# Optimization experiments

Hardware: AMD Instinct MI355X
Metric: run time of the kernel (lower is better)

## Reference

```python
import jax, jax.numpy as jnp
import numpy as np

DELTA_VAR = 0.5
DELTA_DIST = 1.5
VAR_WEIGHT = 1.0
DIST_WEIGHT = 1.0
REG_WEIGHT = 0.001
K = 16  # number of clusters (labels are in [0, K))


def setup_inputs() -> dict:
    key = jax.random.key(0)
    k1, k2 = jax.random.split(key)
    data = jax.random.normal(k1, (32, 512, 1024), dtype=jnp.float32)
    labels = jax.random.randint(k2, (512, 1024), 0, K, dtype=jnp.int32)
    return {"data": data, "labels": labels}


def reference(data, labels):
    D = data.shape[0]
    pts = data.reshape(D, -1).T          # [N, D] per-pixel embeddings
    lab = labels.reshape(-1)             # [N]

    # Per-cluster size and mean (center). All K clusters are present.
    counts = jax.ops.segment_sum(jnp.ones_like(lab, dtype=pts.dtype), lab,
                                 num_segments=K)          # [K]
    sums = jax.ops.segment_sum(pts, lab, num_segments=K)  # [K, D]
    centers = sums / counts[:, None]                      # [K, D]

    # Variance term: sum over all points of hinge(||center - x|| - dv)^2 / K
    diff = centers[lab] - pts                             # [N, D]
    dist = jnp.sqrt(jnp.sum(diff * diff, axis=-1))        # [N]
    var_term = jnp.sum(jnp.maximum(dist - DELTA_VAR, 0.0) ** 2) / K

    # Distance term: ordered pairs i != j of hinge(2*dd - ||ci - cj||)^2
    cd = centers[:, None, :] - centers[None, :, :]        # [K, K, D]
    sq = jnp.sum(cd * cd, axis=-1)                        # [K, K]
    eye = jnp.eye(K, dtype=bool)
    pd = jnp.sqrt(jnp.where(eye, 1.0, sq))                # safe sqrt on diag
    hinge = jnp.where(eye, 0.0, jnp.maximum(2.0 * DELTA_DIST - pd, 0.0) ** 2)
    dist_term = jnp.sum(hinge) / (K * (K - 1))

    # Regularization term: mean center norm
    reg_term = jnp.sum(jnp.sqrt(jnp.sum(centers * centers, axis=-1))) / K

    return VAR_WEIGHT * var_term + DIST_WEIGHT * dist_term + REG_WEIGHT * reg_term
```

## Files before the change

kernel.cpp:

```cpp
#include <hip/hip_runtime.h>


constexpr int KC = 16;
constexpr int DD = 32;
constexpr int NN = 512 * 1024;
constexpr int N4 = NN / 4;
constexpr int CHUNKS = 32;
constexpr int GROUPS_PER_CHUNK = N4 / CHUNKS;
constexpr int K1_ITERS = GROUPS_PER_CHUNK / 256;

constexpr int WS_P  = 0;
constexpr int WS_CP = 16384;

__global__ __launch_bounds__(256) void kA_sums(const float4* __restrict__ data4,
                                               const int4* __restrict__ lab4,
                                               float* __restrict__ ws,
                                               float* __restrict__ out) {
    const int tid = threadIdx.x;
    const int chunk = blockIdx.x;
    const int d = blockIdx.y;
    const bool doCnt = (d == 0);

    if (chunk == 0 && d == 0 && tid == 0) out[0] = 0.f;

    __shared__ float acc[KC * 256];
    __shared__ float cnt[KC * 256];
#pragma unroll
    for (int k = 0; k < KC; ++k) acc[k * 256 + tid] = 0.f;
    if (doCnt) {
#pragma unroll
        for (int k = 0; k < KC; ++k) cnt[k * 256 + tid] = 0.f;
    }
    __syncthreads();

    const int c0 = tid;
    const int c1 = (tid + 64) & 255;
    const int c2 = (tid + 128) & 255;
    const int c3 = (tid + 192) & 255;

    const float4* dplane = data4 + (size_t)d * N4;
    int g = chunk * GROUPS_PER_CHUNK + tid;

    float4 v = dplane[g];
    int4 lb = lab4[g];
    for (int it = 0; it < K1_ITERS; ++it) {
        float4 vn;
        int4 lbn;
        if (it + 1 < K1_ITERS) {
            vn = dplane[g + 256];
            lbn = lab4[g + 256];
        }
        const int i0 = lb.x * 256 + c0;
        const int i1 = lb.y * 256 + c1;
        const int i2 = lb.z * 256 + c2;
        const int i3 = lb.w * 256 + c3;
        const float a0 = acc[i0];
        const float a1 = acc[i1];
        const float a2 = acc[i2];
        const float a3 = acc[i3];
        acc[i0] = a0 + v.x;
        acc[i1] = a1 + v.y;
        acc[i2] = a2 + v.z;
        acc[i3] = a3 + v.w;
        if (doCnt) {
            const float b0 = cnt[i0];
            const float b1 = cnt[i1];
            const float b2 = cnt[i2];
            const float b3 = cnt[i3];
            cnt[i0] = b0 + 1.f;
            cnt[i1] = b1 + 1.f;
            cnt[i2] = b2 + 1.f;
            cnt[i3] = b3 + 1.f;
        }
        v = vn;
        lb = lbn;
        g += 256;
    }
    __syncthreads();

    const int k = tid >> 4, seg = tid & 15;
    float s = 0.f;
#pragma unroll
    for (int i = 0; i < 16; ++i) s += acc[k * 256 + seg * 16 + i];
#pragma unroll
    for (int off = 8; off > 0; off >>= 1) s += __shfl_down(s, off, 16);
    if (seg == 0) ws[WS_P + (k * DD + d) * CHUNKS + chunk] = s;
    if (doCnt) {
        float c = 0.f;
#pragma unroll
        for (int i = 0; i < 16; ++i) c += cnt[k * 256 + seg * 16 + i];
#pragma unroll
        for (int off = 8; off > 0; off >>= 1) c += __shfl_down(c, off, 16);
        if (seg == 0) ws[WS_CP + k * CHUNKS + chunk] = c;
    }
}

__global__ __launch_bounds__(256) void kB_var(const float4* __restrict__ data4,
                                              const int4* __restrict__ lab4,
                                              const float* __restrict__ ws,
                                              float* __restrict__ out) {
    __shared__ float csum[KC * 33];
    __shared__ float ccnt[KC];
    __shared__ float ct2[DD * 32];
    const int tid = threadIdx.x;

    {
        int idx = tid;
        const float* p = ws + WS_P + idx * CHUNKS;
        float s = 0.f;
#pragma unroll
        for (int c = 0; c < CHUNKS; ++c) s += p[c];
        csum[(idx >> 5) * 33 + (idx & 31)] = s;
        idx = tid + 256;
        p = ws + WS_P + idx * CHUNKS;
        s = 0.f;
#pragma unroll
        for (int c = 0; c < CHUNKS; ++c) s += p[c];
        csum[(idx >> 5) * 33 + (idx & 31)] = s;
    }
    if (tid < KC) {
        const float* p = ws + WS_CP + tid * CHUNKS;
        float c = 0.f;
#pragma unroll
        for (int i = 0; i < CHUNKS; ++i) c += p[i];
        ccnt[tid] = c;
    }
    __syncthreads();

    for (int idx = tid; idx < KC * DD; idx += 256) {
        const int k = idx >> 5, d = idx & 31;
        const float c = csum[k * 33 + d] / ccnt[k];
        ct2[d * 32 + k] = c;
        ct2[d * 32 + 16 + k] = c;
    }
    __syncthreads();

    if (blockIdx.x == 0) {
        const int i = tid >> 4, j = tid & 15;
        float val;
        if (i != j) {
            float sq = 0.f;
#pragma unroll
            for (int d = 0; d < DD; ++d) {
                const float df = ct2[d * 32 + i] - ct2[d * 32 + j];
                sq += df * df;
            }
            const float pd = sqrtf(sq);
            const float t = fmaxf(3.0f - pd, 0.f);
            val = t * t * (1.0f / (KC * (KC - 1)));
        } else {
            float s2 = 0.f;
#pragma unroll
            for (int d = 0; d < DD; ++d) s2 += ct2[d * 32 + i] * ct2[d * 32 + i];
            val = sqrtf(s2) * (0.001f / KC);
        }
        __shared__ float red[256];
        red[tid] = val;
        __syncthreads();
        for (int off = 128; off > 0; off >>= 1) {
            if (tid < off) red[tid] += red[tid + off];
            __syncthreads();
        }
        if (tid == 0) atomicAdd(out, red[0]);
        __syncthreads();
    }

    const int g = blockIdx.x * 256 + tid;
    const int4 lb = lab4[g];
    const int dup = (tid & 32) >> 1;
    const int o0 = lb.x + dup, o1 = lb.y + dup, o2 = lb.z + dup, o3 = lb.w + dup;

    float s0 = 0.f, s1 = 0.f, s2 = 0.f, s3 = 0.f;
#pragma unroll 8
    for (int d = 0; d < DD; ++d) {
        const float4 v = data4[(size_t)d * N4 + g];
        const float* ctd = ct2 + d * 32;
        const float d0 = ctd[o0] - v.x; s0 += d0 * d0;
        const float d1 = ctd[o1] - v.y; s1 += d1 * d1;
        const float d2 = ctd[o2] - v.z; s2 += d2 * d2;
        const float d3 = ctd[o3] - v.w; s3 += d3 * d3;
    }
    const float h0 = fmaxf(sqrtf(s0) - 0.5f, 0.f);
    const float h1 = fmaxf(sqrtf(s1) - 0.5f, 0.f);
    const float h2 = fmaxf(sqrtf(s2) - 0.5f, 0.f);
    const float h3 = fmaxf(sqrtf(s3) - 0.5f, 0.f);
    float lsum = h0 * h0 + h1 * h1 + h2 * h2 + h3 * h3;

#pragma unroll
    for (int off = 32; off > 0; off >>= 1) lsum += __shfl_down(lsum, off);
    __shared__ float wred[4];
    if ((tid & 63) == 0) wred[tid >> 6] = lsum;
    __syncthreads();
    if (tid == 0) {
        const float s = wred[0] + wred[1] + wred[2] + wred[3];
        atomicAdd(out, s * (1.0f / KC));
    }
}

extern "C" void kernel_launch(void* const* d_in, const int* in_sizes, int n_in,
                              void* d_out, int out_size, void* d_ws, size_t ws_size,
                              hipStream_t stream) {
    const float4* data4 = (const float4*)d_in[0];
    const int4* lab4 = (const int4*)d_in[1];
    float* out = (float*)d_out;
    float* ws = (float*)d_ws;

    kA_sums<<<dim3(CHUNKS, DD), 256, 0, stream>>>(data4, lab4, ws, out);
    kB_var<<<512, 256, 0, stream>>>(data4, lab4, ws, out);
}
```

Baseline: 111.9 us.

## Split count blocks out, use atomic partial sums, and halve per-block work in variance kernel

Kernel A now uses 64 chunks per dimension and moves label counting into 32 dedicated blocks, which frees the d==0 blocks from the extra count scatter and halves shared memory per block. Partial sums go through global atomics into a padded workspace that is zeroed by a memset, replacing the per-chunk arrays that kernel B had to reduce. Kernel B splits the 32 dimensions across two thread halves that combine through shared memory, doubling the block count so more loads are in flight. The costs are an extra memset launch, atomic contention, and nondeterministic float summation order.

```diff
diff --git a/kernel.cpp b/kernel.cpp
--- a/kernel.cpp
+++ b/kernel.cpp
@@ -5,32 +5,29 @@
 constexpr int DD = 32;
 constexpr int NN = 512 * 1024;
 constexpr int N4 = NN / 4;
-constexpr int CHUNKS = 32;
-constexpr int GROUPS_PER_CHUNK = N4 / CHUNKS;
-constexpr int K1_ITERS = GROUPS_PER_CHUNK / 256;
-
-constexpr int WS_P  = 0;
-constexpr int WS_CP = 16384;
+constexpr int CHUNKS = 64;
+constexpr int GPC = N4 / CHUNKS;
+constexpr int AITERS = GPC / 256;
+constexpr int NDATA = CHUNKS * DD;
+constexpr int NCNT = 32;
+constexpr int CITERS = N4 / NCNT / 256;
+
+constexpr int WS_SUM = 0;
+constexpr int WS_CNT = 8192;
+constexpr int WS_ZERO_FLOATS = 8448;
 
 __global__ __launch_bounds__(256) void kA_sums(const float4* __restrict__ data4,
                                                const int4* __restrict__ lab4,
                                                float* __restrict__ ws,
                                                float* __restrict__ out) {
     const int tid = threadIdx.x;
-    const int chunk = blockIdx.x;
-    const int d = blockIdx.y;
-    const bool doCnt = (d == 0);
-
-    if (chunk == 0 && d == 0 && tid == 0) out[0] = 0.f;
+    const int bid = blockIdx.x;
+
+    if (bid == 0 && tid == 0) out[0] = 0.f;
 
     __shared__ float acc[KC * 256];
-    __shared__ float cnt[KC * 256];
 #pragma unroll
     for (int k = 0; k < KC; ++k) acc[k * 256 + tid] = 0.f;
-    if (doCnt) {
-#pragma unroll
-        for (int k = 0; k < KC; ++k) cnt[k * 256 + tid] = 0.f;
-    }
     __syncthreads();
 
     const int c0 = tid;
@@ -38,60 +35,78 @@
     const int c2 = (tid + 128) & 255;
     const int c3 = (tid + 192) & 255;
 
-    const float4* dplane = data4 + (size_t)d * N4;
-    int g = chunk * GROUPS_PER_CHUNK + tid;
-
-    float4 v = dplane[g];
-    int4 lb = lab4[g];
-    for (int it = 0; it < K1_ITERS; ++it) {
-        float4 vn;
-        int4 lbn;
-        if (it + 1 < K1_ITERS) {
-            vn = dplane[g + 256];
-            lbn = lab4[g + 256];
-        }
-        const int i0 = lb.x * 256 + c0;
-        const int i1 = lb.y * 256 + c1;
-        const int i2 = lb.z * 256 + c2;
-        const int i3 = lb.w * 256 + c3;
-        const float a0 = acc[i0];
-        const float a1 = acc[i1];
-        const float a2 = acc[i2];
-        const float a3 = acc[i3];
-        acc[i0] = a0 + v.x;
-        acc[i1] = a1 + v.y;
-        acc[i2] = a2 + v.z;
-        acc[i3] = a3 + v.w;
-        if (doCnt) {
-            const float b0 = cnt[i0];
-            const float b1 = cnt[i1];
-            const float b2 = cnt[i2];
-            const float b3 = cnt[i3];
-            cnt[i0] = b0 + 1.f;
-            cnt[i1] = b1 + 1.f;
-            cnt[i2] = b2 + 1.f;
-            cnt[i3] = b3 + 1.f;
-        }
-        v = vn;
-        lb = lbn;
-        g += 256;
-    }
-    __syncthreads();
-
-    const int k = tid >> 4, seg = tid & 15;
-    float s = 0.f;
-#pragma unroll
-    for (int i = 0; i < 16; ++i) s += acc[k * 256 + seg * 16 + i];
-#pragma unroll
-    for (int off = 8; off > 0; off >>= 1) s += __shfl_down(s, off, 16);
-    if (seg == 0) ws[WS_P + (k * DD + d) * CHUNKS + chunk] = s;
-    if (doCnt) {
+    if (bid < NDATA) {
+        const int chunk = bid & (CHUNKS - 1);
+        const int d = bid >> 6;
+        const float4* dplane = data4 + (size_t)d * N4;
+        int g = chunk * GPC + tid;
+
+        float4 v = dplane[g];
+        int4 lb = lab4[g];
+        for (int it = 0; it < AITERS; ++it) {
+            float4 vn;
+            int4 lbn;
+            if (it + 1 < AITERS) {
+                vn = dplane[g + 256];
+                lbn = lab4[g + 256];
+            }
+            const int i0 = lb.x * 256 + c0;
+            const int i1 = lb.y * 256 + c1;
+            const int i2 = lb.z * 256 + c2;
+            const int i3 = lb.w * 256 + c3;
+            const float a0 = acc[i0];
+            const float a1 = acc[i1];
+            const float a2 = acc[i2];
+            const float a3 = acc[i3];
+            acc[i0] = a0 + v.x;
+            acc[i1] = a1 + v.y;
+            acc[i2] = a2 + v.z;
+            acc[i3] = a3 + v.w;
+            v = vn;
+            lb = lbn;
+            g += 256;
+        }
+        __syncthreads();
+
+        const int k = tid >> 4, seg = tid & 15;
+        float s = 0.f;
+#pragma unroll
+        for (int i = 0; i < 16; ++i) s += acc[k * 256 + seg * 16 + i];
+#pragma unroll
+        for (int off = 8; off > 0; off >>= 1) s += __shfl_down(s, off, 16);
+        if (seg == 0) atomicAdd(&ws[WS_SUM + (k * DD + d) * 16], s);
+    } else {
+        const int cb = bid - NDATA;
+        int g = cb * (N4 / NCNT) + tid;
+
+        int4 lb = lab4[g];
+        for (int it = 0; it < CITERS; ++it) {
+            int4 lbn;
+            if (it + 1 < CITERS) lbn = lab4[g + 256];
+            const int i0 = lb.x * 256 + c0;
+            const int i1 = lb.y * 256 + c1;
+            const int i2 = lb.z * 256 + c2;
+            const int i3 = lb.w * 256 + c3;
+            const float a0 = acc[i0];
+            const float a1 = acc[i1];
+            const float a2 = acc[i2];
+            const float a3 = acc[i3];
+            acc[i0] = a0 + 1.f;
+            acc[i1] = a1 + 1.f;
+            acc[i2] = a2 + 1.f;
+            acc[i3] = a3 + 1.f;
+            lb = lbn;
+            g += 256;
+        }
+        __syncthreads();
+
+        const int k = tid >> 4, seg = tid & 15;
         float c = 0.f;
 #pragma unroll
-        for (int i = 0; i < 16; ++i) c += cnt[k * 256 + seg * 16 + i];
+        for (int i = 0; i < 16; ++i) c += acc[k * 256 + seg * 16 + i];
 #pragma unroll
         for (int off = 8; off > 0; off >>= 1) c += __shfl_down(c, off, 16);
-        if (seg == 0) ws[WS_CP + k * CHUNKS + chunk] = c;
+        if (seg == 0) atomicAdd(&ws[WS_CNT + k * 16], c);
     }
 }
 
@@ -99,37 +114,20 @@
                                               const int4* __restrict__ lab4,
                                               const float* __restrict__ ws,
                                               float* __restrict__ out) {
-    __shared__ float csum[KC * 33];
+    __shared__ float csum[512];
     __shared__ float ccnt[KC];
     __shared__ float ct2[DD * 32];
+    __shared__ float sh[4][128];
+    __shared__ float wred[4];
     const int tid = threadIdx.x;
 
-    {
-        int idx = tid;
-        const float* p = ws + WS_P + idx * CHUNKS;
-        float s = 0.f;
-#pragma unroll
-        for (int c = 0; c < CHUNKS; ++c) s += p[c];
-        csum[(idx >> 5) * 33 + (idx & 31)] = s;
-        idx = tid + 256;
-        p = ws + WS_P + idx * CHUNKS;
-        s = 0.f;
-#pragma unroll
-        for (int c = 0; c < CHUNKS; ++c) s += p[c];
-        csum[(idx >> 5) * 33 + (idx & 31)] = s;
-    }
-    if (tid < KC) {
-        const float* p = ws + WS_CP + tid * CHUNKS;
-        float c = 0.f;
-#pragma unroll
-        for (int i = 0; i < CHUNKS; ++i) c += p[i];
-        ccnt[tid] = c;
-    }
-    __syncthreads();
-
+    if (tid < KC) ccnt[tid] = ws[WS_CNT + tid * 16];
+    csum[tid] = ws[WS_SUM + tid * 16];
+    csum[tid + 256] = ws[WS_SUM + (tid + 256) * 16];
+    __syncthreads();
     for (int idx = tid; idx < KC * DD; idx += 256) {
         const int k = idx >> 5, d = idx & 31;
-        const float c = csum[k * 33 + d] / ccnt[k];
+        const float c = csum[idx] / ccnt[k];
         ct2[d * 32 + k] = c;
         ct2[d * 32 + 16 + k] = c;
     }
@@ -165,30 +163,45 @@
         __syncthreads();
     }
 
-    const int g = blockIdx.x * 256 + tid;
+    const int t = tid & 127, half = tid >> 7;
+    const int g = blockIdx.x * 128 + t;
     const int4 lb = lab4[g];
     const int dup = (tid & 32) >> 1;
     const int o0 = lb.x + dup, o1 = lb.y + dup, o2 = lb.z + dup, o3 = lb.w + dup;
 
     float s0 = 0.f, s1 = 0.f, s2 = 0.f, s3 = 0.f;
-#pragma unroll 8
-    for (int d = 0; d < DD; ++d) {
-        const float4 v = data4[(size_t)d * N4 + g];
-        const float* ctd = ct2 + d * 32;
+    const int dbase = half * 16;
+#pragma unroll
+    for (int i = 0; i < 16; ++i) {
+        const int dd = dbase + i;
+        const float4 v = data4[(size_t)dd * N4 + g];
+        const float* ctd = ct2 + dd * 32;
         const float d0 = ctd[o0] - v.x; s0 += d0 * d0;
         const float d1 = ctd[o1] - v.y; s1 += d1 * d1;
         const float d2 = ctd[o2] - v.z; s2 += d2 * d2;
         const float d3 = ctd[o3] - v.w; s3 += d3 * d3;
     }
-    const float h0 = fmaxf(sqrtf(s0) - 0.5f, 0.f);
-    const float h1 = fmaxf(sqrtf(s1) - 0.5f, 0.f);
-    const float h2 = fmaxf(sqrtf(s2) - 0.5f, 0.f);
-    const float h3 = fmaxf(sqrtf(s3) - 0.5f, 0.f);
-    float lsum = h0 * h0 + h1 * h1 + h2 * h2 + h3 * h3;
-
+    if (half) {
+        sh[0][t] = s0;
+        sh[1][t] = s1;
+        sh[2][t] = s2;
+        sh[3][t] = s3;
+    }
+    __syncthreads();
+    float lsum = 0.f;
+    if (!half) {
+        s0 += sh[0][t];
+        s1 += sh[1][t];
+        s2 += sh[2][t];
+        s3 += sh[3][t];
+        const float h0 = fmaxf(sqrtf(s0) - 0.5f, 0.f);
+        const float h1 = fmaxf(sqrtf(s1) - 0.5f, 0.f);
+        const float h2 = fmaxf(sqrtf(s2) - 0.5f, 0.f);
+        const float h3 = fmaxf(sqrtf(s3) - 0.5f, 0.f);
+        lsum = h0 * h0 + h1 * h1 + h2 * h2 + h3 * h3;
+    }
 #pragma unroll
     for (int off = 32; off > 0; off >>= 1) lsum += __shfl_down(lsum, off);
-    __shared__ float wred[4];
     if ((tid & 63) == 0) wred[tid >> 6] = lsum;
     __syncthreads();
     if (tid == 0) {
@@ -205,6 +218,7 @@
     float* out = (float*)d_out;
     float* ws = (float*)d_ws;
 
-    kA_sums<<<dim3(CHUNKS, DD), 256, 0, stream>>>(data4, lab4, ws, out);
-    kB_var<<<512, 256, 0, stream>>>(data4, lab4, ws, out);
+    hipMemsetAsync(ws, 0, WS_ZERO_FLOATS * sizeof(float), stream);
+    kA_sums<<<NDATA + NCNT, 256, 0, stream>>>(data4, lab4, ws, out);
+    kB_var<<<N4 / 128, 256, 0, stream>>>(data4, lab4, ws, out);
 }
```

New measurement: 115.7 us. 1.03x slower.
